# Optimization experiments

Hardware: AMD Instinct MI355X
Metric: run time of the kernel (lower is better)

## Reference

```python
import jax, jax.numpy as jnp
import numpy as np

B = 2          # batch size
T2 = 9         # temporal groups (b*t2 = grid_sample batch)
T3 = 27        # t1 // t2
T1 = 243       # t2 * t3
P = 17         # joints
K2 = 9         # kernel_size ** 2
C = 128        # dim_img
CH = [48, 96, 192, 384]
HW = [(96, 72), (48, 36), (24, 18), (12, 9)]
ALPHA = 0.9


def setup_inputs() -> dict:
    key = jax.random.key(0)
    ks = jax.random.split(key, 16)
    inp = {}
    N = B * T2
    for i, (c, (h, w)) in enumerate(zip(CH, HW)):
        inp[f"f{i}"] = jax.random.normal(ks[i], (N, c, h, w), jnp.float32)
    inp["query"] = jax.random.normal(ks[4], (B, T1, P * K2, C), jnp.float32)
    # key holds normalized grid coords in [-1, 1]
    inp["key"] = jax.random.uniform(ks[5], (N, T3, P * K2, 2), jnp.float32) * 2.0 - 1.0
    inp["value"] = jax.random.normal(ks[6], (B, T1, P, C), jnp.float32)
    s = 0.05
    inp["w_off"] = jax.random.normal(ks[7], (2, C), jnp.float32) * s
    inp["b_off"] = jnp.zeros((2,), jnp.float32)
    inp["w_attn"] = jax.random.normal(ks[8], (2, C), jnp.float32) * s
    inp["b_attn"] = jnp.zeros((2,), jnp.float32)
    for i, c in enumerate(CH):
        inp[f"we{i}"] = jax.random.normal(ks[9 + i], (C, c), jnp.float32) * s
        inp[f"be{i}"] = jnp.zeros((C,), jnp.float32)
    inp["conv_w"] = jax.random.normal(ks[13], (C, C, K2), jnp.float32) * s
    inp["conv_b"] = jnp.zeros((C,), jnp.float32)
    return inp


def _grid_sample(img, grid):
    """Bilinear grid_sample, align_corners=False, zero padding.
    img: [N, C, H, W]; grid: [N, Hg, Wg, 2] in [-1,1] (x=width, y=height).
    Returns [N, Hg, Wg, C] (channels-last for the following 1x1 conv)."""
    N, Cin, H, W = img.shape
    gx, gy = grid[..., 0], grid[..., 1]
    ix = ((gx + 1.0) * W - 1.0) * 0.5
    iy = ((gy + 1.0) * H - 1.0) * 0.5
    ix0 = jnp.floor(ix); iy0 = jnp.floor(iy)
    wx1 = ix - ix0; wx0 = 1.0 - wx1
    wy1 = iy - iy0; wy0 = 1.0 - wy1
    bidx = jnp.arange(N)[:, None, None]

    def gather(yy, xx):
        yi = yy.astype(jnp.int32); xi = xx.astype(jnp.int32)
        valid = (yi >= 0) & (yi < H) & (xi >= 0) & (xi < W)
        yc = jnp.clip(yi, 0, H - 1); xc = jnp.clip(xi, 0, W - 1)
        v = img[bidx, :, yc, xc]  # [N, Hg, Wg, C]
        return v * valid[..., None].astype(img.dtype)

    out = (gather(iy0, ix0) * (wy0 * wx0)[..., None]
           + gather(iy0, ix0 + 1.0) * (wy0 * wx1)[..., None]
           + gather(iy0 + 1.0, ix0) * (wy1 * wx0)[..., None]
           + gather(iy0 + 1.0, ix0 + 1.0) * (wy1 * wx1)[..., None])
    return out


def reference(f0, f1, f2, f3, query, key, value,
              w_off, b_off, w_attn, b_attn,
              we0, be0, we1, be1, we2, be2, we3, be3,
              conv_w, conv_b):
    b, t1, p, c = value.shape            # [B, 243, 17, 128]
    t3 = key.shape[1]                    # 27
    t2 = t1 // t3                        # 9

    # learned offsets per query location, squashed by tanh
    off = jnp.tanh(jnp.einsum('btqc,oc->btqo', query, w_off) + b_off)   # [b,t1,153,2]
    # per-joint softmax weights, tiled over the k^2 kernel taps
    aw = jax.nn.softmax(jnp.einsum('btpc,oc->btpo', value, w_attn) + b_attn, axis=-1)  # [b,t1,17,2]
    aw = jnp.tile(aw, (1, 1, K2, 1))                                     # [b,t1,153,2]

    sp = (off * aw).reshape(b * t2, t3, p * K2, 2)
    sampling_positions = key + sp                                        # [b*t2, 27, 153, 2]

    fmaps = (f0, f1, f2, f3)
    ws = (we0, we1, we2, we3)
    bs = (be0, be1, be2, be3)
    feats = []
    for f, w, bb in zip(fmaps, ws, bs):
        g = _grid_sample(f, sampling_positions)                          # [b*t2, 27, 153, C_in]
        e = jnp.einsum('nhwc,oc->nhwo', g, w) + bb                        # 1x1 conv embed -> 128
        feats.append(e.reshape(b, t2 * t3, p * K2, C))                    # [b, 243, 153, 128]
    new_query = jnp.mean(jnp.stack(feats, axis=-2), axis=-2)             # fuse 4 levels
    new_query = (1.0 - ALPHA) * new_query + ALPHA * query

    # grouped-by-position conv1d over the k^2 taps (full-width kernel -> length 1)
    x = new_query.reshape(b, t1, p, K2, c)                               # 'b t (p k) c'
    new_value = jnp.einsum('btpkc,ock->btpo', x, conv_w) + conv_b        # [b, 243, 17, 128]
    return (new_query, new_value, sampling_positions)
```

## Files before the change

kernel.cpp:

```cpp
#include <hip/hip_runtime.h>
#include <hip/hip_bf16.h>

static constexpr int NQ_SIZE = 9517824;
static constexpr int NV_SIZE = 1057536;
static constexpr int NPOS    = 74358;
static constexpr int M_CONV  = 8262;

static constexpr long E0_OFF = 0;
static constexpr long E1_OFF = 15925248;
static constexpr long E2_OFF = E1_OFF + 3981312;
static constexpr long E3_OFF = E2_OFF + 995328;
static constexpr long E_END  = E3_OFF + 248832;

static constexpr int SEG_L3 = 18;
static constexpr int SEG_L2 = SEG_L3 + 72;
static constexpr int SEG_L1 = SEG_L2 + 252;
static constexpr int SEG_L0 = SEG_L1 + 972;
static constexpr int SEG_AW = SEG_L0 + 65;
static constexpr int SEG_CT = SEG_AW + 576;
static constexpr int PREP_GRID = SEG_CT + 1;

typedef __attribute__((ext_vector_type(8))) short short8;
typedef __attribute__((ext_vector_type(4))) float floatx4;

__device__ __forceinline__ float bf2f(unsigned short u) {
    union { unsigned int i; float f; } v; v.i = ((unsigned)u) << 16; return v.f;
}
__device__ __forceinline__ unsigned short f2bf_rne(float f) {
    union { float f; unsigned int i; } v; v.f = f;
    unsigned int u = v.i;
    u += 0x7fffu + ((u >> 16) & 1u);
    return (unsigned short)(u >> 16);
}
__device__ __forceinline__ short8 pack8(const float* t) {
    union { unsigned short u[8]; short8 s; } r;
    #pragma unroll
    for (int i = 0; i < 8; ++i) r.u[i] = f2bf_rne(t[i]);
    return r.s;
}

template<int K, int M, bool FULLM>
__device__ __forceinline__ void proj_body(
    const float* __restrict__ A, const float* __restrict__ W,
    unsigned short* __restrict__ Eo, int m0, int tid,
    unsigned short* __restrict__ shbuf)
{
    constexpr int KC      = (K < 96) ? K : 96;
    constexpr int KCPAD   = (KC + 31) & ~31;
    constexpr int KT      = KCPAD / 32;
    constexpr int NCH     = K / KC;
    constexpr bool NEEDPAD = (KCPAD != KC);

    unsigned short (*Bs)[104] = (unsigned short (*)[104])shbuf;

    const int lane = tid & 63;
    const int wave = tid >> 6;
    const int l15  = lane & 15;
    const int quad = lane >> 4;
    const int mg0  = m0 + wave * 32 + l15;
    const int mg1  = mg0 + 16;
    const bool v0  = FULLM || (mg0 < M);
    const bool v1  = FULLM || (mg1 < M);

    floatx4 acc[2][8];
    #pragma unroll
    for (int f = 0; f < 2; ++f)
        #pragma unroll
        for (int nt = 0; nt < 8; ++nt) acc[f][nt] = (floatx4){0.f, 0.f, 0.f, 0.f};

    const int so  = tid >> 1;
    const int skb = (tid & 1) * (KCPAD / 2);

    #pragma unroll 1
    for (int ch = 0; ch < NCH; ++ch) {
        const int kc = ch * KC;
        if (ch) __syncthreads();

        {
            const float* wp = W + (long)so * K + kc + skb;
            #pragma unroll
            for (int j = 0; j < KCPAD / 2; j += 8) {
                float t8[8];
                #pragma unroll
                for (int i = 0; i < 8; ++i)
                    t8[i] = (!NEEDPAD || (skb + j + i < KC)) ? wp[j + i] : 0.f;
                unsigned short u[8];
                #pragma unroll
                for (int i = 0; i < 8; ++i) u[i] = f2bf_rne(t8[i]);
                *(uint4*)&Bs[so][skb + j] = *(const uint4*)u;
            }
        }
        __syncthreads();

        #pragma unroll
        for (int kt = 0; kt < KT; ++kt) {
            const int kg = kc + kt * 32 + quad * 8;
            const float* ap = A + (long)kg * M + mg0;
            float a0[8], a1[8];
            if (FULLM && (!NEEDPAD || (kg + 8 <= K))) {
                #pragma unroll
                for (int j = 0; j < 8; ++j) {
                    a0[j] = ap[(long)j * M];
                    a1[j] = ap[(long)j * M + 16];
                }
            } else {
                #pragma unroll
                for (int j = 0; j < 8; ++j) {
                    a0[j] = 0.f; a1[j] = 0.f;
                    if (kg + j < K) {
                        if (v0) a0[j] = ap[(long)j * M];
                        if (v1) a1[j] = ap[(long)j * M + 16];
                    }
                }
            }
            short8 af0 = pack8(a0);
            short8 af1 = pack8(a1);
            #pragma unroll
            for (int nt = 0; nt < 8; ++nt) {
                short8 bf = *(const short8*)&Bs[nt * 16 + l15][kt * 32 + quad * 8];
                acc[0][nt] = __builtin_amdgcn_mfma_f32_16x16x32_bf16(af0, bf, acc[0][nt], 0, 0, 0);
                acc[1][nt] = __builtin_amdgcn_mfma_f32_16x16x32_bf16(af1, bf, acc[1][nt], 0, 0, 0);
            }
        }
    }

    __syncthreads();
    #pragma unroll
    for (int f = 0; f < 2; ++f) {
        #pragma unroll
        for (int nt = 0; nt < 8; ++nt) {
            #pragma unroll
            for (int r = 0; r < 4; ++r) {
                int row = wave * 32 + f * 16 + quad * 4 + r;
                shbuf[row * 128 + nt * 16 + l15] = f2bf_rne(acc[f][nt][r]);
            }
        }
    }
    __syncthreads();
    const uint4* sb4 = (const uint4*)shbuf;
    uint4* eo4 = (uint4*)(Eo + (long)m0 * 128);
    #pragma unroll
    for (int j = 0; j < 8; ++j) {
        int off16 = wave * 512 + j * 64 + lane;
        if (FULLM || (m0 + (off16 >> 4) < M))
            eo4[off16] = sb4[off16];
    }
}

__global__ __launch_bounds__(256) void prep_k(
    const float* __restrict__ f0, const float* __restrict__ f1,
    const float* __restrict__ f2, const float* __restrict__ f3,
    const float* __restrict__ we0, const float* __restrict__ we1,
    const float* __restrict__ we2, const float* __restrict__ we3,
    const float* __restrict__ conv_w, unsigned short* __restrict__ convT2,
    const float* __restrict__ value,
    const float* __restrict__ w_attn, const float* __restrict__ b_attn,
    const float* __restrict__ be0, const float* __restrict__ be1,
    const float* __restrict__ be2, const float* __restrict__ be3,
    float* __restrict__ awbuf, float* __restrict__ besum,
    unsigned short* __restrict__ Ebase)
{
    __shared__ unsigned short shbuf[128 * 128];
    const int bid = blockIdx.x;
    const int tid = threadIdx.x;

    if (bid < SEG_L0) {
        if (bid < SEG_L3) {
            int n = bid;
            proj_body<384, 108, false>(f3 + (long)n * 384 * 108, we3,
                Ebase + E3_OFF + (long)n * 108 * 128, 0, tid, shbuf);
        } else if (bid < SEG_L2) {
            int r = bid - SEG_L3; int n = r >> 2, t = r & 3;
            const float* A = f2 + (long)n * 192 * 432;
            unsigned short* Eo = Ebase + E2_OFF + (long)n * 432 * 128;
            if (t < 3) proj_body<192, 432, true >(A, we2, Eo, t * 128, tid, shbuf);
            else       proj_body<192, 432, false>(A, we2, Eo, t * 128, tid, shbuf);
        } else if (bid < SEG_L1) {
            int r = bid - SEG_L2; int n = r / 14, t = r - n * 14;
            const float* A = f1 + (long)n * 96 * 1728;
            unsigned short* Eo = Ebase + E1_OFF + (long)n * 1728 * 128;
            if (t < 13) proj_body<96, 1728, true >(A, we1, Eo, t * 128, tid, shbuf);
            else        proj_body<96, 1728, false>(A, we1, Eo, t * 128, tid, shbuf);
        } else {
            int r = bid - SEG_L1; int n = r / 54, t = r - n * 54;
            proj_body<48, 6912, true>(f0 + (long)n * 48 * 6912, we0,
                Ebase + E0_OFF + (long)n * 6912 * 128, t * 128, tid, shbuf);
        }
    } else if (bid < SEG_AW) {
        int t = (bid - SEG_L0) * 256 + tid;
        if (t < 16524) {
            int rp = t >> 1, o = t & 1;
            const float* vrow = value + (long)rp * 128;
            const float* wrow = w_attn + o * 128;
            float s = 0.f;
            for (int c = 0; c < 128; c += 4) {
                float4 v = *(const float4*)(vrow + c);
                float4 w = *(const float4*)(wrow + c);
                s += v.x * w.x + v.y * w.y + v.z * w.z + v.w * w.w;
            }
            s += b_attn[o];
            float so = __shfl_xor(s, 1);
            float m = fmaxf(s, so);
            float e = __expf(s - m), eo = __expf(so - m);
            awbuf[t] = e / (e + eo);
        }
    } else if (bid < SEG_CT) {
        int idx = (bid - SEG_AW) * 256 + tid;
        if (idx < 147456) {
            int o = idx / 1152, kk = idx - o * 1152;
            int k2 = kk >> 7, c = kk & 127;
            convT2[idx] = f2bf_rne(conv_w[o * 1152 + c * 9 + k2]);
        }
    } else {
        if (tid < 128)
            besum[tid] = be0[tid] + be1[tid] + be2[tid] + be3[tid];
    }
}

__global__ __launch_bounds__(256) void gather_k(
    const unsigned short* __restrict__ Ebase,
    const float* __restrict__ query, const float* __restrict__ key,
    const float* __restrict__ w_off, const float* __restrict__ b_off,
    const float* __restrict__ awbuf, const float* __restrict__ besum,
    float* __restrict__ nq, float* __restrict__ samp)
{
    const int tid = threadIdx.x;
    const int li  = (blockIdx.x & 7) * 581 + (blockIdx.x >> 3);
    const int pos = li * 16 + (tid >> 4);
    if (pos >= NPOS) return;
    const int l16 = tid & 15;
    const int c8  = l16 << 3;

    const int bt1 = pos / 153, q = pos - bt1 * 153;
    const int b  = bt1 / 243, t1 = bt1 - b * 243;
    const int t2 = t1 / 27,  t3 = t1 - t2 * 27;
    const int n  = b * 9 + t2;
    const int p  = q % 17;

    const long qi = (long)pos * 128 + c8;
    const float4 qv0 = *(const float4*)(query + qi);
    const float4 qv1 = *(const float4*)(query + qi + 4);

    float4 w0a = *(const float4*)(w_off + c8);
    float4 w0b = *(const float4*)(w_off + c8 + 4);
    float4 w1a = *(const float4*)(w_off + 128 + c8);
    float4 w1b = *(const float4*)(w_off + 128 + c8 + 4);
    float s0 = qv0.x * w0a.x + qv0.y * w0a.y + qv0.z * w0a.z + qv0.w * w0a.w
             + qv1.x * w0b.x + qv1.y * w0b.y + qv1.z * w0b.z + qv1.w * w0b.w;
    float s1 = qv0.x * w1a.x + qv0.y * w1a.y + qv0.z * w1a.z + qv0.w * w1a.w
             + qv1.x * w1b.x + qv1.y * w1b.y + qv1.z * w1b.z + qv1.w * w1b.w;
    #pragma unroll
    for (int m = 8; m >= 1; m >>= 1) {
        s0 += __shfl_xor(s0, m);
        s1 += __shfl_xor(s1, m);
    }
    const float aw0 = awbuf[(bt1 * 17 + p) * 2];
    const float aw1 = awbuf[(bt1 * 17 + p) * 2 + 1];
    const float off0 = tanhf(s0 + b_off[0]);
    const float off1 = tanhf(s1 + b_off[1]);
    const long kidx = (((long)n * 27 + t3) * 153 + q) * 2;
    const float gx = key[kidx]     + off0 * aw0;
    const float gy = key[kidx + 1] + off1 * aw1;
    if (l16 == 0) *(float2*)(samp + kidx) = (float2){gx, gy};

    float acc[8];
    #pragma unroll
    for (int j = 0; j < 8; ++j) acc[j] = 0.f;
    const long Eoffs[4] = {E0_OFF, E1_OFF, E2_OFF, E3_OFF};
    const int Hs[4] = {96, 48, 24, 12}, Wd[4] = {72, 36, 18, 9};
    #pragma unroll
    for (int l = 0; l < 4; ++l) {
        const int H = Hs[l], W = Wd[l];
        const unsigned short* E = Ebase + Eoffs[l] + (long)n * H * W * 128 + c8;
        float ix = ((gx + 1.f) * (float)W - 1.f) * 0.5f;
        float iy = ((gy + 1.f) * (float)H - 1.f) * 0.5f;
        float fx0 = floorf(ix), fy0 = floorf(iy);
        int x0 = (int)fx0, y0 = (int)fy0;
        int x1 = x0 + 1, y1 = y0 + 1;
        float wx1 = ix - fx0, wx0 = 1.f - wx1;
        float wy1 = iy - fy0, wy0 = 1.f - wy1;
        bool vy0 = (unsigned)y0 < (unsigned)H, vy1 = (unsigned)y1 < (unsigned)H;
        bool vx0 = (unsigned)x0 < (unsigned)W, vx1 = (unsigned)x1 < (unsigned)W;
        float w00 = (vy0 && vx0) ? wy0 * wx0 : 0.f;
        float w01 = (vy0 && vx1) ? wy0 * wx1 : 0.f;
        float w10 = (vy1 && vx0) ? wy1 * wx0 : 0.f;
        float w11 = (vy1 && vx1) ? wy1 * wx1 : 0.f;
        int yc0 = min(max(y0, 0), H - 1), yc1 = min(max(y1, 0), H - 1);
        int xc0 = min(max(x0, 0), W - 1), xc1 = min(max(x1, 0), W - 1);
        short8 v00 = *(const short8*)(E + ((long)yc0 * W + xc0) * 128);
        short8 v01 = *(const short8*)(E + ((long)yc0 * W + xc1) * 128);
        short8 v10 = *(const short8*)(E + ((long)yc1 * W + xc0) * 128);
        short8 v11 = *(const short8*)(E + ((long)yc1 * W + xc1) * 128);
        #pragma unroll
        for (int j = 0; j < 8; ++j) {
            float a = acc[j];
            a = fmaf(w00, bf2f((unsigned short)v00[j]), a);
            a = fmaf(w01, bf2f((unsigned short)v01[j]), a);
            a = fmaf(w10, bf2f((unsigned short)v10[j]), a);
            a = fmaf(w11, bf2f((unsigned short)v11[j]), a);
            acc[j] = a;
        }
    }
    const float4 bs0 = *(const float4*)(besum + c8);
    const float4 bs1 = *(const float4*)(besum + c8 + 4);
    float4 o0, o1;
    o0.x = 0.1f * (0.25f * (acc[0] + bs0.x)) + 0.9f * qv0.x;
    o0.y = 0.1f * (0.25f * (acc[1] + bs0.y)) + 0.9f * qv0.y;
    o0.z = 0.1f * (0.25f * (acc[2] + bs0.z)) + 0.9f * qv0.z;
    o0.w = 0.1f * (0.25f * (acc[3] + bs0.w)) + 0.9f * qv0.w;
    o1.x = 0.1f * (0.25f * (acc[4] + bs1.x)) + 0.9f * qv1.x;
    o1.y = 0.1f * (0.25f * (acc[5] + bs1.y)) + 0.9f * qv1.y;
    o1.z = 0.1f * (0.25f * (acc[6] + bs1.z)) + 0.9f * qv1.z;
    o1.w = 0.1f * (0.25f * (acc[7] + bs1.w)) + 0.9f * qv1.w;
    *(float4*)(nq + qi)     = o0;
    *(float4*)(nq + qi + 4) = o1;
}

__global__ __launch_bounds__(256) void conv_mfma_k(
    const float* __restrict__ nq, const unsigned short* __restrict__ convT2,
    const float* __restrict__ conv_b, float* __restrict__ nv)
{
    __shared__ unsigned short As[32][72];
    __shared__ unsigned short Bs[128][72];

    const int tid  = threadIdx.x;
    const int lane = tid & 63;
    const int wave = tid >> 6;
    const int m0 = blockIdx.x * 32;
    const int l15  = lane & 15;
    const int quad = lane >> 4;

    floatx4 acc[2][2];
    #pragma unroll
    for (int mf = 0; mf < 2; ++mf)
        #pragma unroll
        for (int nt = 0; nt < 2; ++nt) acc[mf][nt] = (floatx4){0.f, 0.f, 0.f, 0.f};

    const int am = tid >> 3;
    const int ak = (tid & 7) << 3;
    const int bn = tid >> 1;
    const int bk = (tid & 1) << 5;

    float4 a0, a1; uint4 bv0, bv1, bv2, bv3;
    auto fetch = [&](int k0) {
        a0 = (float4){0,0,0,0}; a1 = a0;
        int row = m0 + am;
        if (row < M_CONV) {
            a0 = *(const float4*)(nq + (long)row * 1152 + k0 + ak);
            a1 = *(const float4*)(nq + (long)row * 1152 + k0 + ak + 4);
        }
        const unsigned short* bp = convT2 + (long)bn * 1152 + k0 + bk;
        bv0 = *(const uint4*)(bp);
        bv1 = *(const uint4*)(bp + 8);
        bv2 = *(const uint4*)(bp + 16);
        bv3 = *(const uint4*)(bp + 24);
    };
    fetch(0);

    for (int k0 = 0; k0 < 1152; k0 += 64) {
        unsigned short t[8] = {f2bf_rne(a0.x), f2bf_rne(a0.y), f2bf_rne(a0.z), f2bf_rne(a0.w),
                               f2bf_rne(a1.x), f2bf_rne(a1.y), f2bf_rne(a1.z), f2bf_rne(a1.w)};
        *(uint4*)&As[am][ak] = *(const uint4*)t;
        *(uint4*)&Bs[bn][bk]      = bv0;
        *(uint4*)&Bs[bn][bk + 8]  = bv1;
        *(uint4*)&Bs[bn][bk + 16] = bv2;
        *(uint4*)&Bs[bn][bk + 24] = bv3;
        __syncthreads();
        if (k0 + 64 < 1152) fetch(k0 + 64);

        #pragma unroll
        for (int kt = 0; kt < 2; ++kt) {
            short8 af0 = *(const short8*)&As[l15][kt * 32 + quad * 8];
            short8 af1 = *(const short8*)&As[16 + l15][kt * 32 + quad * 8];
            #pragma unroll
            for (int nt = 0; nt < 2; ++nt) {
                short8 bf = *(const short8*)&Bs[wave * 32 + nt * 16 + l15][kt * 32 + quad * 8];
                acc[0][nt] = __builtin_amdgcn_mfma_f32_16x16x32_bf16(af0, bf, acc[0][nt], 0, 0, 0);
                acc[1][nt] = __builtin_amdgcn_mfma_f32_16x16x32_bf16(af1, bf, acc[1][nt], 0, 0, 0);
            }
        }
        __syncthreads();
    }

    #pragma unroll
    for (int nt = 0; nt < 2; ++nt) {
        const int col = wave * 32 + nt * 16 + l15;
        const float bias = conv_b[col];
        #pragma unroll
        for (int mf = 0; mf < 2; ++mf) {
            #pragma unroll
            for (int r = 0; r < 4; ++r) {
                int row = m0 + mf * 16 + quad * 4 + r;
                if (row < M_CONV)
                    nv[(long)row * 128 + col] = acc[mf][nt][r] + bias;
            }
        }
    }
}

extern "C" void kernel_launch(void* const* d_in, const int* in_sizes, int n_in,
                              void* d_out, int out_size, void* d_ws, size_t ws_size,
                              hipStream_t stream) {
    const float* f0     = (const float*)d_in[0];
    const float* f1     = (const float*)d_in[1];
    const float* f2     = (const float*)d_in[2];
    const float* f3     = (const float*)d_in[3];
    const float* query  = (const float*)d_in[4];
    const float* key    = (const float*)d_in[5];
    const float* value  = (const float*)d_in[6];
    const float* w_off  = (const float*)d_in[7];
    const float* b_off  = (const float*)d_in[8];
    const float* w_attn = (const float*)d_in[9];
    const float* b_attn = (const float*)d_in[10];
    const float* we0    = (const float*)d_in[11];
    const float* be0    = (const float*)d_in[12];
    const float* we1    = (const float*)d_in[13];
    const float* be1    = (const float*)d_in[14];
    const float* we2    = (const float*)d_in[15];
    const float* be2    = (const float*)d_in[16];
    const float* we3    = (const float*)d_in[17];
    const float* be3    = (const float*)d_in[18];
    const float* conv_w = (const float*)d_in[19];
    const float* conv_b = (const float*)d_in[20];

    float* out  = (float*)d_out;
    float* nq   = out;
    float* nv   = out + NQ_SIZE;
    float* samp = out + NQ_SIZE + NV_SIZE;

    unsigned short* Ebase  = (unsigned short*)d_ws;
    unsigned short* convT2 = Ebase + E_END;
    float* awbuf = nv;
    float* besum = nv + 16524;

    prep_k<<<PREP_GRID, 256, 0, stream>>>(
        f0, f1, f2, f3, we0, we1, we2, we3, conv_w, convT2,
        value, w_attn, b_attn, be0, be1, be2, be3, awbuf, besum, Ebase);

    gather_k<<<4648, 256, 0, stream>>>(
        Ebase, query, key, w_off, b_off, awbuf, besum, nq, samp);

    conv_mfma_k<<<259, 256, 0, stream>>>(nq, convT2, conv_b, nv);
}
```

Baseline: 214.0 us.

## Compute sampling positions in prep kernel instead of gather kernel

```diff
diff --git a/kernel.cpp b/kernel.cpp
--- a/kernel.cpp
+++ b/kernel.cpp
@@ -13,11 +13,11 @@
 static constexpr long E_END  = E3_OFF + 248832;
 
 static constexpr int SEG_L3 = 18;
-static constexpr int SEG_L2 = SEG_L3 + 72;
+static constexpr int SEG_SP = SEG_L3 + 486;
+static constexpr int SEG_L2 = SEG_SP + 72;
 static constexpr int SEG_L1 = SEG_L2 + 252;
 static constexpr int SEG_L0 = SEG_L1 + 972;
-static constexpr int SEG_AW = SEG_L0 + 65;
-static constexpr int SEG_CT = SEG_AW + 576;
+static constexpr int SEG_CT = SEG_L0 + 576;
 static constexpr int PREP_GRID = SEG_CT + 1;
 
 typedef __attribute__((ext_vector_type(8))) short short8;
@@ -153,24 +153,26 @@
     const float* __restrict__ we0, const float* __restrict__ we1,
     const float* __restrict__ we2, const float* __restrict__ we3,
     const float* __restrict__ conv_w, unsigned short* __restrict__ convT2,
-    const float* __restrict__ value,
+    const float* __restrict__ query, const float* __restrict__ value,
+    const float* __restrict__ key,
+    const float* __restrict__ w_off, const float* __restrict__ b_off,
     const float* __restrict__ w_attn, const float* __restrict__ b_attn,
     const float* __restrict__ be0, const float* __restrict__ be1,
     const float* __restrict__ be2, const float* __restrict__ be3,
-    float* __restrict__ awbuf, float* __restrict__ besum,
+    float* __restrict__ besum, float* __restrict__ samp,
     unsigned short* __restrict__ Ebase)
 {
     __shared__ unsigned short shbuf[128 * 128];
     const int bid = blockIdx.x;
     const int tid = threadIdx.x;
 
-    if (bid < SEG_L0) {
+    if (bid < SEG_L3 || (bid >= SEG_SP && bid < SEG_L0)) {
         if (bid < SEG_L3) {
             int n = bid;
             proj_body<384, 108, false>(f3 + (long)n * 384 * 108, we3,
                 Ebase + E3_OFF + (long)n * 108 * 128, 0, tid, shbuf);
         } else if (bid < SEG_L2) {
-            int r = bid - SEG_L3; int n = r >> 2, t = r & 3;
+            int r = bid - SEG_SP; int n = r >> 2, t = r & 3;
             const float* A = f2 + (long)n * 192 * 432;
             unsigned short* Eo = Ebase + E2_OFF + (long)n * 432 * 128;
             if (t < 3) proj_body<192, 432, true >(A, we2, Eo, t * 128, tid, shbuf);
@@ -186,11 +188,17 @@
             proj_body<48, 6912, true>(f0 + (long)n * 48 * 6912, we0,
                 Ebase + E0_OFF + (long)n * 6912 * 128, t * 128, tid, shbuf);
         }
-    } else if (bid < SEG_AW) {
-        int t = (bid - SEG_L0) * 256 + tid;
-        if (t < 16524) {
-            int rp = t >> 1, o = t & 1;
-            const float* vrow = value + (long)rp * 128;
+    } else if (bid < SEG_SP) {
+        const int bt1 = bid - SEG_L3;
+        const int b  = bt1 / 243, t1 = bt1 - b * 243;
+        const int t2 = t1 / 27,  t3 = t1 - t2 * 27;
+        const int n  = b * 9 + t2;
+        __shared__ float logit[17][2];
+        __shared__ float aw[17][2];
+
+        if (tid < 34) {
+            int p = tid >> 1, o = tid & 1;
+            const float* vrow = value + ((long)bt1 * 17 + p) * 128;
             const float* wrow = w_attn + o * 128;
             float s = 0.f;
             for (int c = 0; c < 128; c += 4) {
@@ -198,14 +206,34 @@
                 float4 w = *(const float4*)(wrow + c);
                 s += v.x * w.x + v.y * w.y + v.z * w.z + v.w * w.w;
             }
-            s += b_attn[o];
-            float so = __shfl_xor(s, 1);
-            float m = fmaxf(s, so);
-            float e = __expf(s - m), eo = __expf(so - m);
-            awbuf[t] = e / (e + eo);
+            logit[p][o] = s + b_attn[o];
+        }
+        __syncthreads();
+        if (tid < 17) {
+            float l0 = logit[tid][0], l1 = logit[tid][1];
+            float mx = fmaxf(l0, l1);
+            float e0 = expf(l0 - mx), e1 = expf(l1 - mx);
+            float inv = 1.f / (e0 + e1);
+            aw[tid][0] = e0 * inv; aw[tid][1] = e1 * inv;
+        }
+        __syncthreads();
+        for (int j = tid; j < 306; j += 256) {
+            int q = j >> 1, o = j & 1;
+            const float* qrow = query + ((long)bt1 * 153 + q) * 128;
+            const float* wrow = w_off + o * 128;
+            float s = 0.f;
+            for (int c = 0; c < 128; c += 4) {
+                float4 v = *(const float4*)(qrow + c);
+                float4 w = *(const float4*)(wrow + c);
+                s += v.x * w.x + v.y * w.y + v.z * w.z + v.w * w.w;
+            }
+            float off = tanhf(s + b_off[o]);
+            float sp = off * aw[q % 17][o];
+            long kidx = (((long)n * 27 + t3) * 153 + q) * 2 + o;
+            samp[kidx] = key[kidx] + sp;
         }
     } else if (bid < SEG_CT) {
-        int idx = (bid - SEG_AW) * 256 + tid;
+        int idx = (bid - SEG_L0) * 256 + tid;
         if (idx < 147456) {
             int o = idx / 1152, kk = idx - o * 1152;
             int k2 = kk >> 7, c = kk & 127;
@@ -219,10 +247,9 @@
 
 __global__ __launch_bounds__(256) void gather_k(
     const unsigned short* __restrict__ Ebase,
-    const float* __restrict__ query, const float* __restrict__ key,
-    const float* __restrict__ w_off, const float* __restrict__ b_off,
-    const float* __restrict__ awbuf, const float* __restrict__ besum,
-    float* __restrict__ nq, float* __restrict__ samp)
+    const float* __restrict__ samp, const float* __restrict__ query,
+    const float* __restrict__ besum,
+    float* __restrict__ nq)
 {
     const int tid = threadIdx.x;
     const int li  = (blockIdx.x & 7) * 581 + (blockIdx.x >> 3);
@@ -235,33 +262,14 @@
     const int b  = bt1 / 243, t1 = bt1 - b * 243;
     const int t2 = t1 / 27,  t3 = t1 - t2 * 27;
     const int n  = b * 9 + t2;
-    const int p  = q % 17;
+
+    const long kidx = (((long)n * 27 + t3) * 153 + q) * 2;
+    const float2 g = *(const float2*)(samp + kidx);
+    const float gx = g.x, gy = g.y;
 
     const long qi = (long)pos * 128 + c8;
     const float4 qv0 = *(const float4*)(query + qi);
     const float4 qv1 = *(const float4*)(query + qi + 4);
-
-    float4 w0a = *(const float4*)(w_off + c8);
-    float4 w0b = *(const float4*)(w_off + c8 + 4);
-    float4 w1a = *(const float4*)(w_off + 128 + c8);
-    float4 w1b = *(const float4*)(w_off + 128 + c8 + 4);
-    float s0 = qv0.x * w0a.x + qv0.y * w0a.y + qv0.z * w0a.z + qv0.w * w0a.w
-             + qv1.x * w0b.x + qv1.y * w0b.y + qv1.z * w0b.z + qv1.w * w0b.w;
-    float s1 = qv0.x * w1a.x + qv0.y * w1a.y + qv0.z * w1a.z + qv0.w * w1a.w
-             + qv1.x * w1b.x + qv1.y * w1b.y + qv1.z * w1b.z + qv1.w * w1b.w;
-    #pragma unroll
-    for (int m = 8; m >= 1; m >>= 1) {
-        s0 += __shfl_xor(s0, m);
-        s1 += __shfl_xor(s1, m);
-    }
-    const float aw0 = awbuf[(bt1 * 17 + p) * 2];
-    const float aw1 = awbuf[(bt1 * 17 + p) * 2 + 1];
-    const float off0 = tanhf(s0 + b_off[0]);
-    const float off1 = tanhf(s1 + b_off[1]);
-    const long kidx = (((long)n * 27 + t3) * 153 + q) * 2;
-    const float gx = key[kidx]     + off0 * aw0;
-    const float gy = key[kidx + 1] + off1 * aw1;
-    if (l16 == 0) *(float2*)(samp + kidx) = (float2){gx, gy};
 
     float acc[8];
     #pragma unroll
@@ -430,15 +438,14 @@
 
     unsigned short* Ebase  = (unsigned short*)d_ws;
     unsigned short* convT2 = Ebase + E_END;
-    float* awbuf = nv;
-    float* besum = nv + 16524;
+    float* besum = nv;
 
     prep_k<<<PREP_GRID, 256, 0, stream>>>(
         f0, f1, f2, f3, we0, we1, we2, we3, conv_w, convT2,
-        value, w_attn, b_attn, be0, be1, be2, be3, awbuf, besum, Ebase);
-
-    gather_k<<<4648, 256, 0, stream>>>(
-        Ebase, query, key, w_off, b_off, awbuf, besum, nq, samp);
+        query, value, key, w_off, b_off, w_attn, b_attn,
+        be0, be1, be2, be3, besum, samp, Ebase);
+
+    gather_k<<<4648, 256, 0, stream>>>(Ebase, samp, query, besum, nq);
 
     conv_mfma_k<<<259, 256, 0, stream>>>(nq, convT2, conv_b, nv);
 }
```

After: 225.7 us. 1.05x slower.
